# Kernel tuning notes

Measured on AMD Instinct MI355X. Metric: run time of the kernel, lower is better.

Reference implementation:

```python
import jax, jax.numpy as jnp
import numpy as np

EPS = 1e-5
N_HEADS = 16

def _bn(x, g, b, m, v):
    # x: (N,C,L); inference-mode batchnorm with running stats
    scale = g * jax.lax.rsqrt(v + EPS)
    return (x - m[None, :, None]) * scale[None, :, None] + b[None, :, None]

def _conv1d(x, w, b, pad):
    # x: (N,C,L), w: (O,I,K) torch layout
    y = jax.lax.conv_general_dilated(x, w, window_strides=(1,), padding=[(pad, pad)],
                                     dimension_numbers=('NCH', 'OIH', 'NCH'))
    return y + b[None, :, None]

def _instance_norm(x):
    m = x.mean(-1, keepdims=True)
    v = x.var(-1, keepdims=True)
    return (x - m) * jax.lax.rsqrt(v + EPS)

def setup_inputs() -> dict:
    key = jax.random.key(0)
    ks = jax.random.split(key, 12)
    C, MID, N, L = 1024, 1024, 4, 1024
    s = 0.02
    d = {
        'x': jax.random.normal(ks[0], (N, C, L), jnp.float32),
        'norm_g': jnp.ones((C,), jnp.float32) + 0.1 * jax.random.normal(ks[1], (C,)),
        'norm_b': 0.1 * jax.random.normal(ks[2], (C,)),
        'norm_m': 0.05 * jax.random.normal(ks[3], (C,)),
        'norm_v': jnp.ones((C,), jnp.float32),
        'wq': s * jax.random.normal(ks[4], (C, C)),
        'wk': s * jax.random.normal(ks[5], (C, C)),
        'wv': s * jax.random.normal(ks[6], (C, C)),
        'wo': s * jax.random.normal(ks[7], (C, C)),
        'cw1': s * jax.random.normal(ks[8], (MID, C, 1)),
        'cb1': jnp.zeros((MID,), jnp.float32),
        'cw2': s * jax.random.normal(ks[9], (MID, MID, 3)),
        'cb2': jnp.zeros((MID,), jnp.float32),
        'cw3': s * jax.random.normal(ks[10], (C, MID, 1)),
        'cb3': jnp.zeros((C,), jnp.float32),
    }
    for i, cdim in [(1, MID), (2, MID), (3, C)]:
        kk = jax.random.split(ks[11], 8)
        d[f'bn{i}_g'] = jnp.ones((cdim,), jnp.float32) + 0.1 * jax.random.normal(kk[2 * i - 2], (cdim,))
        d[f'bn{i}_b'] = 0.1 * jax.random.normal(kk[2 * i - 1], (cdim,))
        d[f'bn{i}_m'] = 0.05 * jax.random.normal(jax.random.fold_in(key, 100 + i), (cdim,))
        d[f'bn{i}_v'] = jnp.ones((cdim,), jnp.float32)
    return d

def _attention(h, wq, wk, wv, wo):
    # h: (N,L,C) ; torch Linear: y = x @ W.T
    N, L, C = h.shape
    dh = C // N_HEADS
    q = (h @ wq.T).reshape(N, L, N_HEADS, dh)
    k = (h @ wk.T).reshape(N, L, N_HEADS, dh)
    v = (h @ wv.T).reshape(N, L, N_HEADS, dh)
    att = jnp.einsum('nqhd,nkhd->nhqk', q, k) / jnp.sqrt(jnp.float32(C))  # note: /sqrt(d_model) as in source
    att = jax.nn.softmax(att, axis=-1)
    o = jnp.einsum('nhqk,nkhd->nqhd', att, v).reshape(N, L, C)
    return o @ wo.T

def _forward(x, norm_g, norm_b, norm_m, norm_v, wq, wk, wv, wo,
             cw1, cb1, bn1_g, bn1_b, bn1_m, bn1_v,
             cw2, cb2, bn2_g, bn2_b, bn2_m, bn2_v,
             cw3, cb3, bn3_g, bn3_b, bn3_m, bn3_v):
    # self-attention branch (dropout is identity in eval)
    h = _bn(x, norm_g, norm_b, norm_m, norm_v).transpose(0, 2, 1)  # (N,L,C)
    h = h + _attention(h, wq, wk, wv, wo)
    h = h.transpose(0, 2, 1)  # (N,C,L)
    # IbnNet (bottleneck conv block + residual + optional InstanceNorm)
    y = jax.nn.relu(_bn(_conv1d(h, cw1, cb1, 0), bn1_g, bn1_b, bn1_m, bn1_v))
    y = jax.nn.relu(_bn(_conv1d(y, cw2, cb2, 1), bn2_g, bn2_b, bn2_m, bn2_v))
    y = _bn(_conv1d(y, cw3, cb3, 0), bn3_g, bn3_b, bn3_m, bn3_v)
    y = jax.nn.relu(_instance_norm(y + h))
    # max_pool1d(kernel=2, stride=2)
    N, C, L = y.shape
    return y.reshape(N, C, L // 2, 2).max(axis=-1)

def reference(x, norm_g, norm_b, norm_m, norm_v, wq, wk, wv, wo,
              cw1, cb1, bn1_g, bn1_b, bn1_m, bn1_v,
              cw2, cb2, bn2_g, bn2_b, bn2_m, bn2_v,
              cw3, cb3, bn3_g, bn3_b, bn3_m, bn3_v):
    return _forward(x, norm_g, norm_b, norm_m, norm_v, wq, wk, wv, wo,
                    cw1, cb1, bn1_g, bn1_b, bn1_m, bn1_v,
                    cw2, cb2, bn2_g, bn2_b, bn2_m, bn2_v,
                    cw3, cb3, bn3_g, bn3_b, bn3_m, bn3_v)
```

## Files before the change

### kernel.cpp

```cpp
#include <hip/hip_runtime.h>
#include <cstdint>
#include <cstddef>


typedef __bf16 bf16_t;
typedef __attribute__((ext_vector_type(8))) __bf16 bf16x8;
typedef __attribute__((ext_vector_type(4))) __bf16 bf16x4;
typedef __attribute__((ext_vector_type(4))) float f32x4;
typedef __attribute__((ext_vector_type(8))) unsigned short u16x8;
typedef __attribute__((address_space(1))) unsigned int gu32;
typedef __attribute__((address_space(3))) unsigned int lu32;

#define EPSF 1e-5f

__device__ __forceinline__ void glds16(const void* g, void* l) {
  __builtin_amdgcn_global_load_lds((gu32*)g, (lu32*)l, 16, 0, 0);
}

__device__ __forceinline__ f32x4 mfma16(bf16x8 a, bf16x8 b, f32x4 c) {
  return __builtin_amdgcn_mfma_f32_16x16x32_bf16(a, b, c, 0, 0, 0);
}

__global__ void bn_consts_k(const float* __restrict__ g, const float* __restrict__ b,
                            const float* __restrict__ m, const float* __restrict__ v,
                            const float* __restrict__ cb,
                            float* __restrict__ sc, float* __restrict__ sh, int C) {
  int i = blockIdx.x * 256 + threadIdx.x;
  if (i < C) {
    float s = g[i] * rsqrtf(v[i] + EPSF);
    sc[i] = s;
    sh[i] = b[i] + ((cb ? cb[i] : 0.f) - m[i]) * s;
  }
}

__global__ __launch_bounds__(256)
void bn_transpose_k(const float* __restrict__ x, const float* __restrict__ sc,
                    const float* __restrict__ sh, float* __restrict__ H0f,
                    bf16_t* __restrict__ H0b) {
  __shared__ float T[32][33];
  const int n = blockIdx.x, c0 = blockIdx.y * 32, l0 = blockIdx.z * 32;
  const int tx = threadIdx.x & 31, ty = threadIdx.x >> 5;
#pragma unroll
  for (int cc = 0; cc < 4; ++cc) {
    int c = c0 + ty + cc * 8;
    float v = x[((size_t)(n * 1024 + c) << 10) + l0 + tx];
    T[ty + cc * 8][tx] = v * sc[c] + sh[c];
  }
  __syncthreads();
#pragma unroll
  for (int cc = 0; cc < 4; ++cc) {
    int l = l0 + ty + cc * 8;
    float v = T[tx][ty + cc * 8];
    size_t idx = ((size_t)(n * 1024 + l) << 10) + c0 + tx;
    H0f[idx] = v;
    H0b[idx] = (bf16_t)v;
  }
}

__global__ void cast_bf16_k(const float* __restrict__ s, bf16_t* __restrict__ d, int n4) {
  int i = blockIdx.x * 256 + threadIdx.x;
  if (i >= n4) return;
  f32x4 v = *(const f32x4*)(s + (size_t)i * 4);
  bf16x4 o;
  o[0] = (bf16_t)v[0]; o[1] = (bf16_t)v[1]; o[2] = (bf16_t)v[2]; o[3] = (bf16_t)v[3];
  *(bf16x4*)(d + (size_t)i * 4) = o;
}

__global__ void pack_w2_k(const float* __restrict__ s, bf16_t* __restrict__ d) {
  int i = blockIdx.x * 256 + threadIdx.x;
  int o = i / 3072;
  int r = i - o * 3072;
  int c = r / 3;
  int k = r - c * 3;
  d[(size_t)o * 3072 + k * 1024 + c] = (bf16_t)s[i];
}

__global__ void build_a2_k(const bf16_t* __restrict__ Y1, bf16_t* __restrict__ A2) {
  int t = blockIdx.x * 256 + threadIdx.x;
  int i = t / 384;
  int qq = t - i * 384;
  int tap = qq >> 7;
  int c8 = (qq & 127) * 8;
  int l = i & 1023;
  int ll = l + tap - 1;
  u16x8 val = {0, 0, 0, 0, 0, 0, 0, 0};
  if ((unsigned)ll < 1024u) val = *(const u16x8*)(Y1 + (size_t)(i + tap - 1) * 1024 + c8);
  *(u16x8*)(A2 + (size_t)i * 3072 + tap * 1024 + c8) = val;
}

__global__ __launch_bounds__(256)
void gemm_nt(const bf16_t* __restrict__ A, const bf16_t* __restrict__ B, int K,
             float alpha, const float* __restrict__ bnScale,
             const float* __restrict__ bnShift, int doRelu,
             const float* __restrict__ resid, float* __restrict__ outF,
             bf16_t* __restrict__ outB, int vtrans) {
  __shared__ __align__(16) bf16_t As[128 * 64];
  __shared__ __align__(16) bf16_t Bs[64 * 64];

  const int bid = blockIdx.x;
  const int idx = bid >> 3;
  const int mt = (bid & 7) * 4 + (idx >> 4);
  const int nt = idx & 15;
  const int tileM = mt * 128, tileN = nt * 64;

  const int tid = threadIdx.x;
  const int lane = tid & 63;
  const int w = tid >> 6, wr = w >> 1, wc = w & 1;
  const int l16 = lane & 15, g = lane >> 4;

  const bf16_t* aSrc[4]; bf16_t* aDst[4];
  const bf16_t* bSrc[2]; bf16_t* bDst[2];
#pragma unroll
  for (int it = 0; it < 4; ++it) {
    int q = it * 256 + tid, r = q >> 3, s = q & 7;
    aSrc[it] = A + (size_t)(tileM + r) * K + ((s ^ (r & 7)) * 8);
    aDst[it] = As + q * 8;
  }
#pragma unroll
  for (int it = 0; it < 2; ++it) {
    int q = it * 256 + tid, r = q >> 3, s = q & 7;
    bSrc[it] = B + (size_t)(tileN + r) * K + ((s ^ (r & 7)) * 8);
    bDst[it] = Bs + q * 8;
  }

  f32x4 acc[4][2];
#pragma unroll
  for (int m = 0; m < 4; ++m)
#pragma unroll
    for (int n = 0; n < 2; ++n) acc[m][n] = {0.f, 0.f, 0.f, 0.f};

  for (int k0 = 0; k0 < K; k0 += 64) {
#pragma unroll
    for (int it = 0; it < 4; ++it) glds16(aSrc[it] + k0, aDst[it]);
#pragma unroll
    for (int it = 0; it < 2; ++it) glds16(bSrc[it] + k0, bDst[it]);
    __syncthreads();
#pragma unroll
    for (int kk = 0; kk < 2; ++kk) {
      bf16x8 af[4], bfr[2];
#pragma unroll
      for (int m = 0; m < 4; ++m) {
        int r = wr * 64 + m * 16 + l16;
        af[m] = *(const bf16x8*)(As + r * 64 + (((kk * 4 + g) ^ (r & 7)) * 8));
      }
#pragma unroll
      for (int n = 0; n < 2; ++n) {
        int r = wc * 32 + n * 16 + l16;
        bfr[n] = *(const bf16x8*)(Bs + r * 64 + (((kk * 4 + g) ^ (r & 7)) * 8));
      }
#pragma unroll
      for (int m = 0; m < 4; ++m)
#pragma unroll
        for (int n = 0; n < 2; ++n) acc[m][n] = mfma16(af[m], bfr[n], acc[m][n]);
    }
    __syncthreads();
  }

#pragma unroll
  for (int m = 0; m < 4; ++m) {
#pragma unroll
    for (int n = 0; n < 2; ++n) {
#pragma unroll
      for (int j = 0; j < 4; ++j) {
        const int gr = tileM + wr * 64 + m * 16 + g * 4 + j;
        const int gc = tileN + wc * 32 + n * 16 + l16;
        float v = acc[m][n][j] * alpha;
        if (bnScale) v = v * bnScale[gc] + bnShift[gc];
        if (resid) v += resid[((size_t)gr << 10) + gc];
        if (doRelu) v = fmaxf(v, 0.f);
        if (outF) outF[((size_t)gr << 10) + gc] = v;
        if (outB) {
          if (vtrans)
            outB[((size_t)(gr >> 10) << 20) + ((size_t)gc << 10) + (gr & 1023)] = (bf16_t)v;
          else
            outB[((size_t)gr << 10) + gc] = (bf16_t)v;
        }
      }
    }
  }
}

__global__ __launch_bounds__(256)
void attn_fwd(const bf16_t* __restrict__ Qb, const bf16_t* __restrict__ Kb,
              const bf16_t* __restrict__ Vt, bf16_t* __restrict__ AO) {
  __shared__ __align__(16) bf16_t Ks[2][64][64];
  __shared__ __align__(16) bf16_t Vs[2][64][64];
  __shared__ __align__(16) bf16_t Ps[4][2][16][64];

  const int bid = blockIdx.x;
  const int xcd = bid & 7, idx = bid >> 3;
  const int head = xcd * 8 + (idx >> 3);
  const int qblk = idx & 7;
  const int n = head >> 4, h = head & 15;

  const int tid = threadIdx.x, lane = tid & 63, w = tid >> 6;
  const int l16 = lane & 15, g = lane >> 4;
  const int qbase = qblk * 128 + w * 32;

  bf16x8 aq[2][2];
#pragma unroll
  for (int s = 0; s < 2; ++s) {
    const size_t qoff = ((size_t)(n * 1024 + qbase + s * 16 + l16) << 10) + h * 64;
    aq[s][0] = *(const bf16x8*)(Qb + qoff + g * 8);
    aq[s][1] = *(const bf16x8*)(Qb + qoff + 32 + g * 8);
  }

  const bf16_t* Khead = Kb + ((size_t)(n * 1024) << 10) + h * 64;
  const bf16_t* Vhead = Vt + ((size_t)n << 20) + ((size_t)(h * 64) << 10);

  f32x4 oa[2][4];
  float psum[2][4];
#pragma unroll
  for (int s = 0; s < 2; ++s)
#pragma unroll
    for (int i = 0; i < 4; ++i) {
      oa[s][i] = {0.f, 0.f, 0.f, 0.f};
      psum[s][i] = 0.f;
    }

#pragma unroll
  for (int it = 0; it < 2; ++it) {
    int q = it * 256 + tid, r = q >> 3, c = q & 7;
    glds16(Khead + ((size_t)r << 10) + ((c ^ (r & 7)) * 8), &Ks[0][r][c * 8]);
    glds16(Vhead + ((size_t)r << 10) + ((c ^ (r & 7)) * 8), &Vs[0][r][c * 8]);
  }
  asm volatile("s_waitcnt vmcnt(0)" ::: "memory");
  __syncthreads();

  int buf = 0;
  for (int t = 0; t < 16; ++t) {
    if (t < 15) {
      const int kv0 = (t + 1) * 64;
#pragma unroll
      for (int it = 0; it < 2; ++it) {
        int q = it * 256 + tid, r = q >> 3, c = q & 7;
        glds16(Khead + ((size_t)(kv0 + r) << 10) + ((c ^ (r & 7)) * 8),
               &Ks[buf ^ 1][r][c * 8]);
        glds16(Vhead + ((size_t)r << 10) + kv0 + ((c ^ (r & 7)) * 8),
               &Vs[buf ^ 1][r][c * 8]);
      }
    }
    bf16x8 kf[8];
#pragma unroll
    for (int nf = 0; nf < 4; ++nf) {
      const int r = nf * 16 + l16;
      kf[2 * nf]     = *(const bf16x8*)(&Ks[buf][r][((g)     ^ (r & 7)) * 8]);
      kf[2 * nf + 1] = *(const bf16x8*)(&Ks[buf][r][((4 + g) ^ (r & 7)) * 8]);
    }
#pragma unroll
    for (int s = 0; s < 2; ++s) {
      f32x4 sc[4];
#pragma unroll
      for (int nf = 0; nf < 4; ++nf) sc[nf] = {0.f, 0.f, 0.f, 0.f};
#pragma unroll
      for (int nf = 0; nf < 4; ++nf) {
        sc[nf] = mfma16(aq[s][0], kf[2 * nf], sc[nf]);
        sc[nf] = mfma16(aq[s][1], kf[2 * nf + 1], sc[nf]);
      }
#pragma unroll
      for (int nf = 0; nf < 4; ++nf)
#pragma unroll
        for (int j = 0; j < 4; ++j) {
          float p = __expf(sc[nf][j]);
          psum[s][j] += p;
          const int row = g * 4 + j;
          const int ch = (nf * 2 + (l16 >> 3)) ^ (row & 7);
          Ps[w][s][row][ch * 8 + (l16 & 7)] = (bf16_t)p;
        }
    }
    bf16x8 vf[8];
#pragma unroll
    for (int nf = 0; nf < 4; ++nf) {
      const int r = nf * 16 + l16;
      vf[2 * nf]     = *(const bf16x8*)(&Vs[buf][r][((g)     ^ (r & 7)) * 8]);
      vf[2 * nf + 1] = *(const bf16x8*)(&Vs[buf][r][((4 + g) ^ (r & 7)) * 8]);
    }
#pragma unroll
    for (int s = 0; s < 2; ++s)
#pragma unroll
      for (int kk = 0; kk < 2; ++kk) {
        const int ch = (kk * 4 + g) ^ (l16 & 7);
        bf16x8 pa = *(const bf16x8*)(&Ps[w][s][l16][ch * 8]);
#pragma unroll
        for (int nf = 0; nf < 4; ++nf)
          oa[s][nf] = mfma16(pa, vf[2 * nf + kk], oa[s][nf]);
      }
    asm volatile("s_waitcnt vmcnt(0)" ::: "memory");
    __syncthreads();
    buf ^= 1;
  }

#pragma unroll
  for (int s = 0; s < 2; ++s)
#pragma unroll
    for (int j = 0; j < 4; ++j) {
      float sv = psum[s][j];
#pragma unroll
      for (int o = 1; o < 16; o <<= 1) sv += __shfl_xor(sv, o);
      psum[s][j] = sv;
    }
#pragma unroll
  for (int s = 0; s < 2; ++s)
#pragma unroll
    for (int nf = 0; nf < 4; ++nf)
#pragma unroll
      for (int j = 0; j < 4; ++j) {
        const int q = qbase + s * 16 + g * 4 + j;
        AO[((size_t)(n * 1024 + q) << 10) + h * 64 + nf * 16 + l16] =
            (bf16_t)(oa[s][nf][j] / psum[s][j]);
      }
}

__global__ void in_stats_k(const float* __restrict__ Z, float* __restrict__ ps,
                           float* __restrict__ pq) {
  const int n = blockIdx.x, c = blockIdx.y * 256 + threadIdx.x, z = blockIdx.z;
  float s = 0.f, s2 = 0.f;
  for (int i = 0; i < 128; ++i) {
    float v = Z[((size_t)(n * 1024 + z * 128 + i) << 10) + c];
    s += v;
    s2 += v * v;
  }
  ps[z * 4096 + n * 1024 + c] = s;
  pq[z * 4096 + n * 1024 + c] = s2;
}

__global__ __launch_bounds__(256)
void finalize_k(const float* __restrict__ Z, const float* __restrict__ ps,
                const float* __restrict__ pq, float* __restrict__ out) {
  __shared__ float T[32][33];
  const int n = blockIdx.x, c0 = blockIdx.y * 32, j0 = blockIdx.z * 32;
  const int tx = threadIdx.x & 31, ty = threadIdx.x >> 5;
  const int c = c0 + tx;
  float s = 0.f, q = 0.f;
#pragma unroll
  for (int z = 0; z < 8; ++z) {
    s += ps[z * 4096 + n * 1024 + c];
    q += pq[z * 4096 + n * 1024 + c];
  }
  const float mean = s * (1.f / 1024.f);
  const float var = q * (1.f / 1024.f) - mean * mean;
  const float rstd = rsqrtf(var + EPSF);
#pragma unroll
  for (int jj = 0; jj < 4; ++jj) {
    const int j = j0 + ty + jj * 8;
    float a = Z[((size_t)(n * 1024 + 2 * j) << 10) + c];
    float b = Z[((size_t)(n * 1024 + 2 * j + 1) << 10) + c];
    float v = (fmaxf(a, b) - mean) * rstd;
    T[ty + jj * 8][tx] = fmaxf(v, 0.f);
  }
  __syncthreads();
#pragma unroll
  for (int jj = 0; jj < 4; ++jj)
    out[((size_t)(n * 1024 + c0 + ty + jj * 8) << 9) + j0 + tx] = T[tx][ty + jj * 8];
}

extern "C" void kernel_launch(void* const* d_in, const int* in_sizes, int n_in,
                              void* d_out, int out_size, void* d_ws, size_t ws_size,
                              hipStream_t stream) {
  const float* x      = (const float*)d_in[0];
  const float* norm_g = (const float*)d_in[1];
  const float* norm_b = (const float*)d_in[2];
  const float* norm_m = (const float*)d_in[3];
  const float* norm_v = (const float*)d_in[4];
  const float* wq     = (const float*)d_in[5];
  const float* wk     = (const float*)d_in[6];
  const float* wv     = (const float*)d_in[7];
  const float* wo     = (const float*)d_in[8];
  const float* cw1    = (const float*)d_in[9];
  const float* cb1    = (const float*)d_in[10];
  const float* cw2    = (const float*)d_in[11];
  const float* cb2    = (const float*)d_in[12];
  const float* cw3    = (const float*)d_in[13];
  const float* cb3    = (const float*)d_in[14];
  const float* bn1_g  = (const float*)d_in[15];
  const float* bn1_b  = (const float*)d_in[16];
  const float* bn1_m  = (const float*)d_in[17];
  const float* bn1_v  = (const float*)d_in[18];
  const float* bn2_g  = (const float*)d_in[19];
  const float* bn2_b  = (const float*)d_in[20];
  const float* bn2_m  = (const float*)d_in[21];
  const float* bn2_v  = (const float*)d_in[22];
  const float* bn3_g  = (const float*)d_in[23];
  const float* bn3_b  = (const float*)d_in[24];
  const float* bn3_m  = (const float*)d_in[25];
  const float* bn3_v  = (const float*)d_in[26];

  char* ws = (char*)d_ws;
  const size_t MB = 1024 * 1024;
  float*  H0f = (float*)(ws);
  float*  Zf  = H0f;
  float*  H2f = (float*)(ws + 16 * MB);
  bf16_t* H0b = (bf16_t*)(ws + 32 * MB);
  bf16_t* Y2  = H0b;
  bf16_t* Qb  = (bf16_t*)(ws + 40 * MB);
  bf16_t* Kb  = (bf16_t*)(ws + 48 * MB);
  bf16_t* Vt  = (bf16_t*)(ws + 56 * MB);
  bf16_t* A2  = Qb;
  bf16_t* AOb = (bf16_t*)(ws + 64 * MB);
  bf16_t* Y1  = AOb;
  bf16_t* H2b = (bf16_t*)(ws + 72 * MB);
  bf16_t* wqb = (bf16_t*)(ws + 80 * MB);
  bf16_t* wkb = (bf16_t*)(ws + 82 * MB);
  bf16_t* wvb = (bf16_t*)(ws + 84 * MB);
  bf16_t* wob = (bf16_t*)(ws + 86 * MB);
  bf16_t* w1b = (bf16_t*)(ws + 88 * MB);
  bf16_t* w3b = (bf16_t*)(ws + 90 * MB);
  bf16_t* w2b = (bf16_t*)(ws + 92 * MB);
  float* sc0 = (float*)(ws + 98 * MB);
  float* sh0 = sc0 + 1024;
  float* sc1 = sc0 + 2048;
  float* sh1 = sc0 + 3072;
  float* sc2 = sc0 + 4096;
  float* sh2 = sc0 + 5120;
  float* sc3 = sc0 + 6144;
  float* sh3 = sc0 + 7168;
  float* ps  = sc0 + 8192;
  float* pq  = ps + 32768;

  bn_consts_k<<<4, 256, 0, stream>>>(norm_g, norm_b, norm_m, norm_v, nullptr, sc0, sh0, 1024);
  bn_consts_k<<<4, 256, 0, stream>>>(bn1_g, bn1_b, bn1_m, bn1_v, cb1, sc1, sh1, 1024);
  bn_consts_k<<<4, 256, 0, stream>>>(bn2_g, bn2_b, bn2_m, bn2_v, cb2, sc2, sh2, 1024);
  bn_consts_k<<<4, 256, 0, stream>>>(bn3_g, bn3_b, bn3_m, bn3_v, cb3, sc3, sh3, 1024);

  bn_transpose_k<<<dim3(4, 32, 32), 256, 0, stream>>>(x, sc0, sh0, H0f, H0b);

  cast_bf16_k<<<1024, 256, 0, stream>>>(wq, wqb, 262144);
  cast_bf16_k<<<1024, 256, 0, stream>>>(wk, wkb, 262144);
  cast_bf16_k<<<1024, 256, 0, stream>>>(wv, wvb, 262144);
  cast_bf16_k<<<1024, 256, 0, stream>>>(wo, wob, 262144);
  cast_bf16_k<<<1024, 256, 0, stream>>>(cw1, w1b, 262144);
  cast_bf16_k<<<1024, 256, 0, stream>>>(cw3, w3b, 262144);
  pack_w2_k<<<12288, 256, 0, stream>>>(cw2, w2b);

  gemm_nt<<<512, 256, 0, stream>>>(H0b, wqb, 1024, 0.03125f, nullptr, nullptr, 0, nullptr, nullptr, Qb, 0);
  gemm_nt<<<512, 256, 0, stream>>>(H0b, wkb, 1024, 1.f, nullptr, nullptr, 0, nullptr, nullptr, Kb, 0);
  gemm_nt<<<512, 256, 0, stream>>>(H0b, wvb, 1024, 1.f, nullptr, nullptr, 0, nullptr, nullptr, Vt, 1);

  attn_fwd<<<512, 256, 0, stream>>>(Qb, Kb, Vt, AOb);

  gemm_nt<<<512, 256, 0, stream>>>(AOb, wob, 1024, 1.f, nullptr, nullptr, 0, H0f, H2f, H2b, 0);
  gemm_nt<<<512, 256, 0, stream>>>(H2b, w1b, 1024, 1.f, sc1, sh1, 1, nullptr, nullptr, Y1, 0);
  build_a2_k<<<6144, 256, 0, stream>>>(Y1, A2);
  gemm_nt<<<512, 256, 0, stream>>>(A2, w2b, 3072, 1.f, sc2, sh2, 1, nullptr, nullptr, Y2, 0);
  gemm_nt<<<512, 256, 0, stream>>>(Y2, w3b, 1024, 1.f, sc3, sh3, 0, H2f, Zf, nullptr, 0);

  in_stats_k<<<dim3(4, 4, 8), 256, 0, stream>>>(Zf, ps, pq);
  finalize_k<<<dim3(4, 32, 16), 256, 0, stream>>>(Zf, ps, pq, (float*)d_out);
}
```

Measured before the change: 289.7 us.

## Double-buffer GEMM LDS loads, fuse QKV projections and weight casts

The GEMM kernel now double-buffers its LDS tiles, prefetching the next K-slice while MFMAs run on the current one, so load latency no longer sits between compute steps. The three Q/K/V projection GEMMs are merged into a single launch over a 3072-wide N, with per-section scaling and V written transposed in the epilogue. The six weight cast kernels are merged into one launch. The fused QKV path assumes wqb, wkb and wvb are contiguous and that Qb, Kb and Vt sit at fixed offsets from each other. Doubling LDS per block may reduce occupancy.

```diff
diff --git a/kernel.cpp b/kernel.cpp
--- a/kernel.cpp
+++ b/kernel.cpp
@@ -57,9 +57,23 @@
   }
 }
 
-__global__ void cast_bf16_k(const float* __restrict__ s, bf16_t* __restrict__ d, int n4) {
-  int i = blockIdx.x * 256 + threadIdx.x;
-  if (i >= n4) return;
+__global__ void cast6_k(const float* __restrict__ s0, const float* __restrict__ s1,
+                        const float* __restrict__ s2, const float* __restrict__ s3,
+                        const float* __restrict__ s4, const float* __restrict__ s5,
+                        bf16_t* __restrict__ d0, bf16_t* __restrict__ d1,
+                        bf16_t* __restrict__ d2, bf16_t* __restrict__ d3,
+                        bf16_t* __restrict__ d4, bf16_t* __restrict__ d5) {
+  const int b = blockIdx.x, which = b >> 10;
+  const int i = (b & 1023) * 256 + threadIdx.x;
+  const float* s; bf16_t* d;
+  switch (which) {
+    case 0: s = s0; d = d0; break;
+    case 1: s = s1; d = d1; break;
+    case 2: s = s2; d = d2; break;
+    case 3: s = s3; d = d3; break;
+    case 4: s = s4; d = d4; break;
+    default: s = s5; d = d5; break;
+  }
   f32x4 v = *(const f32x4*)(s + (size_t)i * 4);
   bf16x4 o;
   o[0] = (bf16_t)v[0]; o[1] = (bf16_t)v[1]; o[2] = (bf16_t)v[2]; o[3] = (bf16_t)v[3];
@@ -90,17 +104,16 @@
 
 __global__ __launch_bounds__(256)
 void gemm_nt(const bf16_t* __restrict__ A, const bf16_t* __restrict__ B, int K,
-             float alpha, const float* __restrict__ bnScale,
+             int nNT, int qkv, float alpha, const float* __restrict__ bnScale,
              const float* __restrict__ bnShift, int doRelu,
              const float* __restrict__ resid, float* __restrict__ outF,
-             bf16_t* __restrict__ outB, int vtrans) {
-  __shared__ __align__(16) bf16_t As[128 * 64];
-  __shared__ __align__(16) bf16_t Bs[64 * 64];
+             bf16_t* __restrict__ outB) {
+  __shared__ __align__(16) bf16_t As[2][128 * 64];
+  __shared__ __align__(16) bf16_t Bs[2][64 * 64];
 
   const int bid = blockIdx.x;
-  const int idx = bid >> 3;
-  const int mt = (bid & 7) * 4 + (idx >> 4);
-  const int nt = idx & 15;
+  const int wg = (bid & 7) * (gridDim.x >> 3) + (bid >> 3);
+  const int mt = wg / nNT, nt = wg - mt * nNT;
   const int tileM = mt * 128, tileN = nt * 64;
 
   const int tid = threadIdx.x;
@@ -108,19 +121,17 @@
   const int w = tid >> 6, wr = w >> 1, wc = w & 1;
   const int l16 = lane & 15, g = lane >> 4;
 
-  const bf16_t* aSrc[4]; bf16_t* aDst[4];
-  const bf16_t* bSrc[2]; bf16_t* bDst[2];
+  const bf16_t* aSrc[4];
+  const bf16_t* bSrc[2];
 #pragma unroll
   for (int it = 0; it < 4; ++it) {
     int q = it * 256 + tid, r = q >> 3, s = q & 7;
     aSrc[it] = A + (size_t)(tileM + r) * K + ((s ^ (r & 7)) * 8);
-    aDst[it] = As + q * 8;
   }
 #pragma unroll
   for (int it = 0; it < 2; ++it) {
     int q = it * 256 + tid, r = q >> 3, s = q & 7;
     bSrc[it] = B + (size_t)(tileN + r) * K + ((s ^ (r & 7)) * 8);
-    bDst[it] = Bs + q * 8;
   }
 
   f32x4 acc[4][2];
@@ -129,24 +140,34 @@
 #pragma unroll
     for (int n = 0; n < 2; ++n) acc[m][n] = {0.f, 0.f, 0.f, 0.f};
 
+#pragma unroll
+  for (int it = 0; it < 4; ++it) glds16(aSrc[it], &As[0][(it * 256 + tid) * 8]);
+#pragma unroll
+  for (int it = 0; it < 2; ++it) glds16(bSrc[it], &Bs[0][(it * 256 + tid) * 8]);
+  __syncthreads();
+
+  int buf = 0;
   for (int k0 = 0; k0 < K; k0 += 64) {
-#pragma unroll
-    for (int it = 0; it < 4; ++it) glds16(aSrc[it] + k0, aDst[it]);
-#pragma unroll
-    for (int it = 0; it < 2; ++it) glds16(bSrc[it] + k0, bDst[it]);
-    __syncthreads();
+    if (k0 + 64 < K) {
+#pragma unroll
+      for (int it = 0; it < 4; ++it)
+        glds16(aSrc[it] + k0 + 64, &As[buf ^ 1][(it * 256 + tid) * 8]);
+#pragma unroll
+      for (int it = 0; it < 2; ++it)
+        glds16(bSrc[it] + k0 + 64, &Bs[buf ^ 1][(it * 256 + tid) * 8]);
+    }
 #pragma unroll
     for (int kk = 0; kk < 2; ++kk) {
       bf16x8 af[4], bfr[2];
 #pragma unroll
       for (int m = 0; m < 4; ++m) {
         int r = wr * 64 + m * 16 + l16;
-        af[m] = *(const bf16x8*)(As + r * 64 + (((kk * 4 + g) ^ (r & 7)) * 8));
+        af[m] = *(const bf16x8*)(&As[buf][r * 64 + (((kk * 4 + g) ^ (r & 7)) * 8)]);
       }
 #pragma unroll
       for (int n = 0; n < 2; ++n) {
         int r = wc * 32 + n * 16 + l16;
-        bfr[n] = *(const bf16x8*)(Bs + r * 64 + (((kk * 4 + g) ^ (r & 7)) * 8));
+        bfr[n] = *(const bf16x8*)(&Bs[buf][r * 64 + (((kk * 4 + g) ^ (r & 7)) * 8)]);
       }
 #pragma unroll
       for (int m = 0; m < 4; ++m)
@@ -154,6 +175,7 @@
         for (int n = 0; n < 2; ++n) acc[m][n] = mfma16(af[m], bfr[n], acc[m][n]);
     }
     __syncthreads();
+    buf ^= 1;
   }
 
 #pragma unroll
@@ -164,16 +186,21 @@
       for (int j = 0; j < 4; ++j) {
         const int gr = tileM + wr * 64 + m * 16 + g * 4 + j;
         const int gc = tileN + wc * 32 + n * 16 + l16;
-        float v = acc[m][n][j] * alpha;
-        if (bnScale) v = v * bnScale[gc] + bnShift[gc];
-        if (resid) v += resid[((size_t)gr << 10) + gc];
-        if (doRelu) v = fmaxf(v, 0.f);
-        if (outF) outF[((size_t)gr << 10) + gc] = v;
-        if (outB) {
-          if (vtrans)
-            outB[((size_t)(gr >> 10) << 20) + ((size_t)gc << 10) + (gr & 1023)] = (bf16_t)v;
+        if (qkv) {
+          const int which = gc >> 10, c = gc & 1023;
+          float v = acc[m][n][j] * (which == 0 ? 0.03125f : 1.f);
+          if (which == 2)
+            outB[8388608 + ((size_t)(gr >> 10) << 20) + ((size_t)c << 10) + (gr & 1023)] =
+                (bf16_t)v;
           else
-            outB[((size_t)gr << 10) + gc] = (bf16_t)v;
+            outB[(size_t)which * 4194304 + ((size_t)gr << 10) + c] = (bf16_t)v;
+        } else {
+          float v = acc[m][n][j] * alpha;
+          if (bnScale) v = v * bnScale[gc] + bnShift[gc];
+          if (resid) v += resid[((size_t)gr << 10) + gc];
+          if (doRelu) v = fmaxf(v, 0.f);
+          if (outF) outF[((size_t)gr << 10) + gc] = v;
+          if (outB) outB[((size_t)gr << 10) + gc] = (bf16_t)v;
         }
       }
     }
@@ -424,25 +451,24 @@
 
   bn_transpose_k<<<dim3(4, 32, 32), 256, 0, stream>>>(x, sc0, sh0, H0f, H0b);
 
-  cast_bf16_k<<<1024, 256, 0, stream>>>(wq, wqb, 262144);
-  cast_bf16_k<<<1024, 256, 0, stream>>>(wk, wkb, 262144);
-  cast_bf16_k<<<1024, 256, 0, stream>>>(wv, wvb, 262144);
-  cast_bf16_k<<<1024, 256, 0, stream>>>(wo, wob, 262144);
-  cast_bf16_k<<<1024, 256, 0, stream>>>(cw1, w1b, 262144);
-  cast_bf16_k<<<1024, 256, 0, stream>>>(cw3, w3b, 262144);
+  cast6_k<<<6144, 256, 0, stream>>>(wq, wk, wv, wo, cw1, cw3,
+                                    wqb, wkb, wvb, wob, w1b, w3b);
   pack_w2_k<<<12288, 256, 0, stream>>>(cw2, w2b);
 
-  gemm_nt<<<512, 256, 0, stream>>>(H0b, wqb, 1024, 0.03125f, nullptr, nullptr, 0, nullptr, nullptr, Qb, 0);
-  gemm_nt<<<512, 256, 0, stream>>>(H0b, wkb, 1024, 1.f, nullptr, nullptr, 0, nullptr, nullptr, Kb, 0);
-  gemm_nt<<<512, 256, 0, stream>>>(H0b, wvb, 1024, 1.f, nullptr, nullptr, 0, nullptr, nullptr, Vt, 1);
+  gemm_nt<<<1536, 256, 0, stream>>>(H0b, wqb, 1024, 48, 1, 1.f, nullptr, nullptr, 0,
+                                    nullptr, nullptr, Qb);
 
   attn_fwd<<<512, 256, 0, stream>>>(Qb, Kb, Vt, AOb);
 
-  gemm_nt<<<512, 256, 0, stream>>>(AOb, wob, 1024, 1.f, nullptr, nullptr, 0, H0f, H2f, H2b, 0);
-  gemm_nt<<<512, 256, 0, stream>>>(H2b, w1b, 1024, 1.f, sc1, sh1, 1, nullptr, nullptr, Y1, 0);
+  gemm_nt<<<512, 256, 0, stream>>>(AOb, wob, 1024, 16, 0, 1.f, nullptr, nullptr, 0,
+                                   H0f, H2f, H2b);
+  gemm_nt<<<512, 256, 0, stream>>>(H2b, w1b, 1024, 16, 0, 1.f, sc1, sh1, 1,
+                                   nullptr, nullptr, Y1);
   build_a2_k<<<6144, 256, 0, stream>>>(Y1, A2);
-  gemm_nt<<<512, 256, 0, stream>>>(A2, w2b, 3072, 1.f, sc2, sh2, 1, nullptr, nullptr, Y2, 0);
-  gemm_nt<<<512, 256, 0, stream>>>(Y2, w3b, 1024, 1.f, sc3, sh3, 0, H2f, Zf, nullptr, 0);
+  gemm_nt<<<512, 256, 0, stream>>>(A2, w2b, 3072, 16, 0, 1.f, sc2, sh2, 1,
+                                   nullptr, nullptr, Y2);
+  gemm_nt<<<512, 256, 0, stream>>>(Y2, w3b, 1024, 16, 0, 1.f, sc3, sh3, 0,
+                                   H2f, Zf, nullptr);
 
   in_stats_k<<<dim3(4, 4, 8), 256, 0, stream>>>(Zf, ps, pq);
   finalize_k<<<dim3(4, 32, 16), 256, 0, stream>>>(Zf, ps, pq, (float*)d_out);
```

Measured after the change: 265.0 us. 8.5% less time.
